# Kernel tuning notes

Measured on AMD Instinct MI355X. Metric: run time of the kernel, lower is better.

## Reference

```python
import jax, jax.numpy as jnp
import numpy as np

K_NN = 8        # neighbors
RADIUS = 0.1    # neighbor distance cutoff


def setup_inputs() -> dict:
    key = jax.random.key(0)
    k1, k2 = jax.random.split(key)
    B, N, KS = 2, 8192, 16  # batch, points, mask slots
    pc = jax.random.uniform(k1, (B, N, 3), dtype=jnp.float32)
    mask = jax.random.uniform(k2, (B, N, KS), dtype=jnp.float32)
    return {"pc": pc, "mask": mask}


def _knn(k, pc):
    # squared pairwise distances via gemm: (B,N,N)
    sq = jnp.sum(pc * pc, axis=-1)
    d2 = sq[:, :, None] + sq[:, None, :] - 2.0 * jnp.einsum("bnd,bmd->bnm", pc, pc)
    d2 = jnp.maximum(d2, 0.0)
    neg_d2, idx = jax.lax.top_k(-d2, k)          # k smallest distances
    dist = jnp.sqrt(jnp.maximum(-neg_d2, 0.0))   # (B,N,k) euclidean
    return dist, idx


def reference(pc, mask):
    # mask: (B,N,KS) -> (B,KS,N)
    mask_t = jnp.transpose(mask, (0, 2, 1))
    dist, idx = _knn(K_NN, pc)                   # (B,N,k) each
    # replace out-of-radius neighbors with the self index (nearest = self)
    self_idx = idx[:, :, :1]                     # (B,N,1)
    idx = jnp.where(dist > RADIUS, self_idx, idx)
    idx = jax.lax.stop_gradient(idx)
    # grouping_operation: (B,KS,N) gathered at (B,N,k) -> (B,KS,N,k)
    nn_mask = jax.vmap(lambda f, i: f[:, i])(mask_t, idx)
    # loss_norm=1: L1 norm over mask-slot dim (dim=1), mean over k, mean overall
    diff = mask_t[:, :, :, None] - nn_mask       # (B,KS,N,k)
    loss = jnp.sum(jnp.abs(diff), axis=1).mean(axis=-1)  # (B,N)
    return loss.mean()
```

## Files before the change

### kernel.cpp

```cpp
#include <hip/hip_runtime.h>

#define BATCH 2
#define NPTS  8192
#define KS    16
#define KNN   8
#define R2LOOSE 0.0101f
#define KEYMASK 0xFFFFE000u
#define NCELL   1000
#define CSTRIDE 1024

#define QB       64
#define NWAVE    8
#define NTHREADS 512
#define CAP      32
#define NBLK     (BATCH * NPTS / QB)

__device__ __forceinline__ int cell_of(float x, float y, float z) {
    int cx = (int)(x * 10.0f); cx = cx > 9 ? 9 : cx;
    int cy = (int)(y * 10.0f); cy = cy > 9 ? 9 : cy;
    int cz = (int)(z * 10.0f); cz = cz > 9 ? 9 : cz;
    return (cx * 10 + cy) * 10 + cz;
}

__global__ void count_kernel(const float* __restrict__ pc, int* cfill) {
    const int i = blockIdx.x * 1024 + threadIdx.x;
    const float x = pc[3 * i], y = pc[3 * i + 1], z = pc[3 * i + 2];
    const int b = i >> 13;
    atomicAdd(&cfill[b * CSTRIDE + cell_of(x, y, z)], 1);
}

__global__ __launch_bounds__(1024) void scan_kernel(int* cfill, int* cstart,
                                                    float* out) {
    __shared__ int arr[1024];
    const int b = blockIdx.x, t = threadIdx.x;
    if (b == 0 && t == 0) out[0] = 0.0f;
    const int cnt = cfill[b * CSTRIDE + t];
    arr[t] = cnt;
    __syncthreads();
    for (int off = 1; off < 1024; off <<= 1) {
        const int v = (t >= off) ? arr[t - off] : 0;
        __syncthreads();
        arr[t] += v;
        __syncthreads();
    }
    const int excl = arr[t] - cnt;
    cstart[b * CSTRIDE + t] = excl;
    cfill[b * CSTRIDE + t]  = excl;
}

__global__ void scatter_kernel(const float* __restrict__ pc,
                               float4* __restrict__ cs,
                               int* __restrict__ sidx, int* cfill) {
    const int i = blockIdx.x * 1024 + threadIdx.x;
    const float x = pc[3 * i], y = pc[3 * i + 1], z = pc[3 * i + 2];
    const int b = i >> 13;
    const float sq = fmaf(z, z, fmaf(y, y, x * x));
    const int pos = atomicAdd(&cfill[b * CSTRIDE + cell_of(x, y, z)], 1);
    cs[b * NPTS + pos]   = make_float4(x, y, z, -0.5f * sq);
    sidx[b * NPTS + pos] = i & (NPTS - 1);
}

__global__ __launch_bounds__(512) void knn_loss_kernel(
    const float4* __restrict__ cs,
    const int*    __restrict__ sidx,
    const int*    __restrict__ cstart,
    const float*  __restrict__ mask,
    float* __restrict__ out)
{
    __shared__ unsigned sbuf[CAP * NTHREADS];
    __shared__ int      fidx[QB * KNN];
    __shared__ int      qid[QB];
    __shared__ float    red[NWAVE];

    const int t = threadIdx.x;
    const int q = t & (QB - 1);
    const int s = t >> 6;
    const int su = __builtin_amdgcn_readfirstlane(s);
    const int blk = blockIdx.x;
    const int b  = blk >> 7;
    const int q0 = (blk & 127) * QB;
    const int qpos = q0 + q;

    const float4* csb = cs + b * NPTS;
    const float4 qc = csb[qpos];
    const int    qi = sidx[b * NPTS + qpos];
    if (s == 0) qid[q] = qi;

    const float qx = qc.x, qy = qc.y, qz = qc.z;
    const float qs = -2.0f * qc.w;
    const float negthr = (qs - R2LOOSE) * 0.5f;
    const unsigned SENT = (__float_as_uint(R2LOOSE) & KEYMASK) | 0x1FFFu;

    int lex = cell_of(qx, qy, qz);
    int cmn = lex, cmx = lex;
#pragma unroll
    for (int off = 32; off; off >>= 1) {
        cmn = min(cmn, __shfl_xor(cmn, off));
        cmx = max(cmx, __shfl_xor(cmx, off));
    }
    const int cfirst = __builtin_amdgcn_readfirstlane(cmn);
    const int clast  = __builtin_amdgcn_readfirstlane(cmx);

    int lo0 = cfirst - 111, h0 = clast - 89;
    int lo1 = cfirst - 11,  h1 = clast + 11;
    int lo2 = cfirst + 89,  h2 = clast + 111;
    lo0 = min(max(lo0, 0), 1000);
    lo1 = min(max(lo1, 0), 1000);
    lo2 = min(max(lo2, 0), 1000);
    int hp0 = min(max(h0 + 1, 0), 1000);
    int hp1 = min(max(h1 + 1, 0), 1000);
    int hp2 = min(max(h2 + 1, 0), 1000);
    lo1 = max(lo1, hp0);
    lo2 = max(lo2, hp1);

    const int* csp = cstart + b * CSTRIDE;
    const int P0 = csp[lo0], E0 = csp[hp0];
    const int P1 = csp[lo1], E1 = csp[hp1];
    const int P2 = csp[lo2], E2 = csp[hp2];
    const int L0 = max(0, E0 - P0);
    const int L1 = max(0, E1 - P1);
    const int L2 = max(0, E2 - P2);

    int cnt = 0;
    auto EVAL = [&](const float4& c, int spos) {
        const float tt = fmaf(c.x, qx, fmaf(c.y, qy, fmaf(c.z, qz, c.w)));
        const float d2 = fmaxf(fmaf(-2.0f, tt, qs), 0.0f);
        const unsigned key =
            (__float_as_uint(d2) & KEYMASK) | (unsigned)spos;
        const int slot = cnt < (CAP - 1) ? cnt : (CAP - 1);
        sbuf[slot * NTHREADS + t] = key;
        cnt += (tt >= negthr) ? 1 : 0;
    };
    auto SCAN = [&](int P, int L) {
        int j = (su * L) >> 3;
        const int e = ((su + 1) * L) >> 3;
        for (; j + 4 <= e; j += 4) {
            const float4 c0 = csb[P + j];
            const float4 c1 = csb[P + j + 1];
            const float4 c2 = csb[P + j + 2];
            const float4 c3 = csb[P + j + 3];
            EVAL(c0, P + j);     EVAL(c1, P + j + 1);
            EVAL(c2, P + j + 2); EVAL(c3, P + j + 3);
        }
        for (; j < e; ++j) { const float4 c0 = csb[P + j]; EVAL(c0, P + j); }
    };
    SCAN(P0, L0);
    SCAN(P1, L1);
    SCAN(P2, L2);

    unsigned md[KNN];
#pragma unroll
    for (int k = 0; k < KNN; ++k) md[k] = SENT;
    const int m = cnt < CAP ? cnt : CAP;
    for (int k = 0; k < m; ++k) {
        unsigned ky = sbuf[k * NTHREADS + t];
#pragma unroll
        for (int i = 0; i < KNN; ++i) {
            const unsigned mn = min(ky, md[i]);
            const unsigned mx = max(ky, md[i]);
            md[i] = mn; ky = mx;
        }
    }
    __syncthreads();

    {
        uint4* bp = (uint4*)&sbuf[t * KNN];
        bp[0] = make_uint4(md[0], md[1], md[2], md[3]);
        bp[1] = make_uint4(md[4], md[5], md[6], md[7]);
    }
    __syncthreads();

    if (s == 0) {
        for (int l = 1; l < NWAVE; ++l) {
            const uint4* lp = (const uint4*)&sbuf[(l * QB + q) * KNN];
            const uint4 r0 = lp[0], r1 = lp[1];
            const unsigned tk[8] = {r0.x, r0.y, r0.z, r0.w,
                                    r1.x, r1.y, r1.z, r1.w};
#pragma unroll
            for (int k = 0; k < 8; ++k) {
                unsigned ky = tk[k];
                if (ky < md[KNN - 1]) {
#pragma unroll
                    for (int i = 0; i < KNN; ++i) {
                        const unsigned mn = min(ky, md[i]);
                        const unsigned mx = max(ky, md[i]);
                        md[i] = mn; ky = mx;
                    }
                }
            }
        }
#pragma unroll
        for (int k = 0; k < KNN; ++k) {
            const unsigned ky = md[k];
            int nb;
            if (ky >= SENT) {
                nb = qi;
            } else {
                const int sp = (int)(ky & 0x1FFFu);
                const float4 cc = csb[sp];
                const float dx = cc.x - qx;
                const float dy = cc.y - qy;
                const float dz = cc.z - qz;
                const float d2 = fmaf(dx, dx, fmaf(dy, dy, dz * dz));
                nb = (sqrtf(d2) > 0.1f) ? qi : sidx[b * NPTS + sp];
            }
            fidx[q * KNN + k] = nb;
        }
    }
    __syncthreads();

    const int q2 = t >> 3;
    const int j2 = t & 7;
    const int qg = qid[q2];
    const int nb = fidx[q2 * KNN + j2];
    const float* mrow = mask + ((size_t)b * NPTS + qg) * KS;
    const float* nrow = mask + ((size_t)b * NPTS + nb) * KS;
    float acc = 0.0f;
#pragma unroll
    for (int c = 0; c < KS; c += 4) {
        const float4 a = *(const float4*)(mrow + c);
        const float4 v = *(const float4*)(nrow + c);
        acc += fabsf(a.x - v.x) + fabsf(a.y - v.y) +
               fabsf(a.z - v.z) + fabsf(a.w - v.w);
    }

#pragma unroll
    for (int off = 32; off > 0; off >>= 1) acc += __shfl_down(acc, off);
    if ((t & 63) == 0) red[s] = acc;
    __syncthreads();
    if (t == 0) {
        float sum = 0.0f;
#pragma unroll
        for (int i = 0; i < NWAVE; ++i) sum += red[i];
        atomicAdd(out, sum * (1.0f / (BATCH * NPTS * KNN)));
    }
}

extern "C" void kernel_launch(void* const* d_in, const int* in_sizes, int n_in,
                              void* d_out, int out_size, void* d_ws, size_t ws_size,
                              hipStream_t stream) {
    const float* pc   = (const float*)d_in[0];
    const float* mask = (const float*)d_in[1];
    float* out = (float*)d_out;

    float4* cs     = (float4*)d_ws;
    int*    sidx   = (int*)((char*)d_ws + 262144);
    int*    cstart = (int*)((char*)d_ws + 327680);
    int*    cfill  = (int*)((char*)d_ws + 335872);

    hipMemsetAsync(cfill, 0, 2 * CSTRIDE * sizeof(int), stream);
    hipLaunchKernelGGL(count_kernel,   dim3(16), dim3(1024), 0, stream, pc, cfill);
    hipLaunchKernelGGL(scan_kernel,    dim3(2),  dim3(1024), 0, stream,
                       cfill, cstart, out);
    hipLaunchKernelGGL(scatter_kernel, dim3(16), dim3(1024), 0, stream,
                       pc, cs, sidx, cfill);
    hipLaunchKernelGGL(knn_loss_kernel, dim3(NBLK), dim3(512), 0, stream,
                       cs, sidx, cstart, mask, out);
}
```

Before: 87.58 us.

## Fuse binning and kNN into one cooperative kernel with wave-broadcast candidate scan

Result: slower. 115.7 us (+32.1%).

```diff
diff --git a/kernel.cpp b/kernel.cpp
--- a/kernel.cpp
+++ b/kernel.cpp
@@ -1,4 +1,6 @@
 #include <hip/hip_runtime.h>
+#include <hip/hip_cooperative_groups.h>
+namespace cg = cooperative_groups;
 
 #define BATCH 2
 #define NPTS  8192
@@ -22,61 +24,93 @@
     return (cx * 10 + cy) * 10 + cz;
 }
 
-__global__ void count_kernel(const float* __restrict__ pc, int* cfill) {
-    const int i = blockIdx.x * 1024 + threadIdx.x;
-    const float x = pc[3 * i], y = pc[3 * i + 1], z = pc[3 * i + 2];
-    const int b = i >> 13;
-    atomicAdd(&cfill[b * CSTRIDE + cell_of(x, y, z)], 1);
-}
-
-__global__ __launch_bounds__(1024) void scan_kernel(int* cfill, int* cstart,
-                                                    float* out) {
-    __shared__ int arr[1024];
-    const int b = blockIdx.x, t = threadIdx.x;
-    if (b == 0 && t == 0) out[0] = 0.0f;
-    const int cnt = cfill[b * CSTRIDE + t];
-    arr[t] = cnt;
-    __syncthreads();
-    for (int off = 1; off < 1024; off <<= 1) {
-        const int v = (t >= off) ? arr[t - off] : 0;
-        __syncthreads();
-        arr[t] += v;
-        __syncthreads();
-    }
-    const int excl = arr[t] - cnt;
-    cstart[b * CSTRIDE + t] = excl;
-    cfill[b * CSTRIDE + t]  = excl;
-}
-
-__global__ void scatter_kernel(const float* __restrict__ pc,
-                               float4* __restrict__ cs,
-                               int* __restrict__ sidx, int* cfill) {
-    const int i = blockIdx.x * 1024 + threadIdx.x;
-    const float x = pc[3 * i], y = pc[3 * i + 1], z = pc[3 * i + 2];
-    const int b = i >> 13;
-    const float sq = fmaf(z, z, fmaf(y, y, x * x));
-    const int pos = atomicAdd(&cfill[b * CSTRIDE + cell_of(x, y, z)], 1);
-    cs[b * NPTS + pos]   = make_float4(x, y, z, -0.5f * sq);
-    sidx[b * NPTS + pos] = i & (NPTS - 1);
-}
-
-__global__ __launch_bounds__(512) void knn_loss_kernel(
-    const float4* __restrict__ cs,
-    const int*    __restrict__ sidx,
-    const int*    __restrict__ cstart,
-    const float*  __restrict__ mask,
-    float* __restrict__ out)
+__device__ __forceinline__ float bcastf(float v, int j) {
+    return __uint_as_float((unsigned)__builtin_amdgcn_readlane(
+        (int)__float_as_uint(v), j));
+}
+__device__ __forceinline__ int bcasti(int v, int j) {
+    return __builtin_amdgcn_readlane(v, j);
+}
+
+__global__ __launch_bounds__(512) void knn_fused_kernel(
+    const float* __restrict__ pc,
+    const float* __restrict__ mask,
+    float4* __restrict__ cs,
+    int*    __restrict__ sidx,
+    int*    __restrict__ cstart,
+    float*  __restrict__ out)
 {
     __shared__ unsigned sbuf[CAP * NTHREADS];
     __shared__ int      fidx[QB * KNN];
     __shared__ int      qid[QB];
     __shared__ float    red[NWAVE];
 
-    const int t = threadIdx.x;
-    const int q = t & (QB - 1);
-    const int s = t >> 6;
+    const int t   = threadIdx.x;
+    const int blk = blockIdx.x;
+
+    if (blk < BATCH) {
+        int* hist = (int*)sbuf;
+        int* part = (int*)sbuf + 1024;
+        hist[t] = 0; hist[t + 512] = 0;
+        if (blk == 0 && t == 0) out[0] = 0.0f;
+        __syncthreads();
+
+        const float4* pv = (const float4*)(pc + (size_t)blk * NPTS * 3);
+        float px[16], py[16], pz[16];
+        int   cc[16];
+#pragma unroll
+        for (int u = 0; u < 4; ++u) {
+            const int i4 = t + u * 512;
+            const float4 f0 = pv[3 * i4];
+            const float4 f1 = pv[3 * i4 + 1];
+            const float4 f2 = pv[3 * i4 + 2];
+            px[4*u+0] = f0.x; py[4*u+0] = f0.y; pz[4*u+0] = f0.z;
+            px[4*u+1] = f0.w; py[4*u+1] = f1.x; pz[4*u+1] = f1.y;
+            px[4*u+2] = f1.z; py[4*u+2] = f1.w; pz[4*u+2] = f2.x;
+            px[4*u+3] = f2.y; py[4*u+3] = f2.z; pz[4*u+3] = f2.w;
+        }
+#pragma unroll
+        for (int k = 0; k < 16; ++k) {
+            cc[k] = cell_of(px[k], py[k], pz[k]);
+            atomicAdd(&hist[cc[k]], 1);
+        }
+        __syncthreads();
+
+        const int a0 = hist[2 * t], a1 = hist[2 * t + 1];
+        const int psum = a0 + a1;
+        part[t] = psum;
+        __syncthreads();
+        for (int off = 1; off < 512; off <<= 1) {
+            const int v = (t >= off) ? part[t - off] : 0;
+            __syncthreads();
+            part[t] += v;
+            __syncthreads();
+        }
+        const int excl = part[t] - psum;
+        cstart[blk * CSTRIDE + 2 * t]     = excl;
+        cstart[blk * CSTRIDE + 2 * t + 1] = excl + a0;
+        __syncthreads();
+        hist[2 * t] = excl; hist[2 * t + 1] = excl + a0;
+        __syncthreads();
+
+#pragma unroll
+        for (int u = 0; u < 4; ++u) {
+#pragma unroll
+            for (int k = 0; k < 4; ++k) {
+                const int m2 = 4 * u + k;
+                const int pos = atomicAdd(&hist[cc[m2]], 1);
+                const float x = px[m2], y = py[m2], z = pz[m2];
+                const float sq = fmaf(z, z, fmaf(y, y, x * x));
+                cs[blk * NPTS + pos]   = make_float4(x, y, z, -0.5f * sq);
+                sidx[blk * NPTS + pos] = 4 * (t + u * 512) + k;
+            }
+        }
+    }
+    cg::this_grid().sync();
+
+    const int q  = t & (QB - 1);
+    const int s  = t >> 6;
     const int su = __builtin_amdgcn_readfirstlane(s);
-    const int blk = blockIdx.x;
     const int b  = blk >> 7;
     const int q0 = (blk & 127) * QB;
     const int qpos = q0 + q;
@@ -120,33 +154,50 @@
     const int L0 = max(0, E0 - P0);
     const int L1 = max(0, E1 - P1);
     const int L2 = max(0, E2 - P2);
+    const int C  = L0 + L1 + L2;
 
     int cnt = 0;
-    auto EVAL = [&](const float4& c, int spos) {
-        const float tt = fmaf(c.x, qx, fmaf(c.y, qy, fmaf(c.z, qz, c.w)));
-        const float d2 = fmaxf(fmaf(-2.0f, tt, qs), 0.0f);
-        const unsigned key =
-            (__float_as_uint(d2) & KEYMASK) | (unsigned)spos;
-        const int slot = cnt < (CAP - 1) ? cnt : (CAP - 1);
-        sbuf[slot * NTHREADS + t] = key;
-        cnt += (tt >= negthr) ? 1 : 0;
-    };
-    auto SCAN = [&](int P, int L) {
-        int j = (su * L) >> 3;
-        const int e = ((su + 1) * L) >> 3;
-        for (; j + 4 <= e; j += 4) {
-            const float4 c0 = csb[P + j];
-            const float4 c1 = csb[P + j + 1];
-            const float4 c2 = csb[P + j + 2];
-            const float4 c3 = csb[P + j + 3];
-            EVAL(c0, P + j);     EVAL(c1, P + j + 1);
-            EVAL(c2, P + j + 2); EVAL(c3, P + j + 3);
-        }
-        for (; j < e; ++j) { const float4 c0 = csb[P + j]; EVAL(c0, P + j); }
-    };
-    SCAN(P0, L0);
-    SCAN(P1, L1);
-    SCAN(P2, L2);
+    {
+        const int vlo = (su * C) >> 3;
+        const int vhi = ((su + 1) * C) >> 3;
+        auto FLAT2SP = [&](int fi) {
+            fi = min(fi, C - 1);
+            int sp = P0 + fi;
+            sp = (fi >= L0)      ? (P1 + (fi - L0))      : sp;
+            sp = (fi >= L0 + L1) ? (P2 + (fi - L0 - L1)) : sp;
+            return sp;
+        };
+        if (vhi > vlo) {
+            int spv = FLAT2SP(vlo + q);
+            float4 c = csb[spv];
+            for (int g = vlo; g < vhi; g += QB) {
+                const int nj = min(QB, vhi - g);
+                const int gn = g + QB;
+                int spn = spv; float4 cn = c;
+                if (gn < vhi) { spn = FLAT2SP(gn + q); cn = csb[spn]; }
+#pragma unroll
+                for (int j = 0; j < QB; ++j) {
+                    if (j >= nj) break;
+                    const float sx = bcastf(c.x, j);
+                    const float sy = bcastf(c.y, j);
+                    const float sz = bcastf(c.z, j);
+                    const float sw = bcastf(c.w, j);
+                    const int  ssp = bcasti(spv, j);
+                    const float tt = fmaf(sx, qx,
+                                     fmaf(sy, qy, fmaf(sz, qz, sw)));
+                    if (tt >= negthr) {
+                        const float d2 = fmaxf(fmaf(-2.0f, tt, qs), 0.0f);
+                        const unsigned key =
+                            (__float_as_uint(d2) & KEYMASK) | (unsigned)ssp;
+                        const int slot = cnt < (CAP - 1) ? cnt : (CAP - 1);
+                        sbuf[slot * NTHREADS + t] = key;
+                        ++cnt;
+                    }
+                }
+                spv = spn; c = cn;
+            }
+        }
+    }
 
     unsigned md[KNN];
 #pragma unroll
@@ -217,9 +268,9 @@
     const float* nrow = mask + ((size_t)b * NPTS + nb) * KS;
     float acc = 0.0f;
 #pragma unroll
-    for (int c = 0; c < KS; c += 4) {
-        const float4 a = *(const float4*)(mrow + c);
-        const float4 v = *(const float4*)(nrow + c);
+    for (int c2 = 0; c2 < KS; c2 += 4) {
+        const float4 a = *(const float4*)(mrow + c2);
+        const float4 v = *(const float4*)(nrow + c2);
         acc += fabsf(a.x - v.x) + fabsf(a.y - v.y) +
                fabsf(a.z - v.z) + fabsf(a.w - v.w);
     }
@@ -246,14 +297,9 @@
     float4* cs     = (float4*)d_ws;
     int*    sidx   = (int*)((char*)d_ws + 262144);
     int*    cstart = (int*)((char*)d_ws + 327680);
-    int*    cfill  = (int*)((char*)d_ws + 335872);
-
-    hipMemsetAsync(cfill, 0, 2 * CSTRIDE * sizeof(int), stream);
-    hipLaunchKernelGGL(count_kernel,   dim3(16), dim3(1024), 0, stream, pc, cfill);
-    hipLaunchKernelGGL(scan_kernel,    dim3(2),  dim3(1024), 0, stream,
-                       cfill, cstart, out);
-    hipLaunchKernelGGL(scatter_kernel, dim3(16), dim3(1024), 0, stream,
-                       pc, cs, sidx, cfill);
-    hipLaunchKernelGGL(knn_loss_kernel, dim3(NBLK), dim3(512), 0, stream,
-                       cs, sidx, cstart, mask, out);
-}
+
+    void* args[] = {(void*)&pc, (void*)&mask, (void*)&cs,
+                    (void*)&sidx, (void*)&cstart, (void*)&out};
+    hipLaunchCooperativeKernel((void*)knn_fused_kernel, dim3(NBLK),
+                               dim3(NTHREADS), args, 0, stream);
+}
```
